# Kernel optimization log

Hardware: AMD Instinct MI355X
Metric: run time of the kernel (lower is better)

Reference implementation:

```python
import jax, jax.numpy as jnp
import numpy as np

KS = 5
STRIDE = 1


def extract_patches(x, ks, s):
    # TF tf.image.extract_patches ordering: (row, col, channel) flattened
    B, H, W, C = x.shape
    oh = (H - ks) // s + 1
    ow = (W - ks) // s + 1
    cols = [x[:, i:i + (oh - 1) * s + 1:s, j:j + (ow - 1) * s + 1:s, :]
            for i in range(ks) for j in range(ks)]
    p = jnp.stack(cols, axis=3)  # [B, oh, ow, ks*ks, C]
    return p.reshape(B, oh * ow, ks * ks * C)


def setup_inputs() -> dict:
    key = jax.random.key(0)
    k1, k2, k3 = jax.random.split(key, 3)
    B, H, W, C, K = 32, 14, 14, 32, 64
    mu_in = jax.random.normal(k1, (B, H, W, C), dtype=jnp.float32)
    Sigma_in = jax.random.uniform(k2, (B, H * W, H * W, C), dtype=jnp.float32)
    w_mu = 0.05 * jax.random.normal(k3, (KS, KS, C, K), dtype=jnp.float32)
    w_sigma = jnp.full((K,), -2.2, dtype=jnp.float32)
    return {"mu_in": mu_in, "Sigma_in": Sigma_in, "w_mu": w_mu, "w_sigma": w_sigma}


def reference(mu_in, Sigma_in, w_mu, w_sigma):
    B, H, W, C = mu_in.shape
    ks = w_mu.shape[0]
    K = w_mu.shape[-1]
    s = STRIDE

    # mean path: standard conv2d, NHWC / HWIO
    mu_out = jax.lax.conv_general_dilated(
        mu_in, w_mu, (s, s), 'VALID',
        dimension_numbers=('NHWC', 'HWIO', 'NHWC'))

    # diag of Sigma_in over the two N dims: [B,N,N,C] -> [B,C,N] -> [B,H,W,C]
    diag_sigma = jnp.diagonal(Sigma_in, axis1=1, axis2=2)           # [B,C,N]
    diag_sigma = jnp.transpose(diag_sigma, (0, 2, 1)).reshape(B, H, W, C)

    dsg = extract_patches(diag_sigma, ks, s)                        # [B,P,M]
    P = dsg.shape[1]

    mu_cov_sq = (w_mu * w_mu).reshape(-1, K)                        # [M,K]
    v1 = dsg @ mu_cov_sq                                            # [B,P,K]

    sp = jnp.log1p(jnp.exp(w_sigma))                                # softplus, [K]
    tr = jnp.sum(dsg, axis=2, keepdims=True)                        # [B,P,1]
    diag_vals = v1 + sp[None, None, :] * tr                         # [B,P,K] (trace1 + mu_wT_sigmags_mu_w diags)

    mu_p = extract_patches(mu_in, ks, s)                            # [B,P,M]
    G = jnp.einsum('bpm,bqm->bpq', mu_p, mu_p)                      # [B,P,P]

    Sigma_out = sp[None, None, None, :] * G[..., None]              # [B,P,P,K]
    ip = jnp.arange(P)
    Sigma_out = Sigma_out.at[:, ip, ip, :].add(diag_vals)

    Sigma_out = jnp.where(jnp.isnan(Sigma_out), 0.0, Sigma_out)
    Sigma_out = jnp.where(jnp.isinf(Sigma_out), 0.0, Sigma_out)

    # TF set_diag acts on the LAST two dims ([P,K] inner matrices) -- reproduce exactly
    m = min(P, K)
    ii = jnp.arange(m)
    Sigma_out = Sigma_out.at[:, :, ii, ii].set(jnp.abs(Sigma_out[:, :, ii, ii]))
    return mu_out, Sigma_out
```

## Files before the change

kernel.cpp:

```cpp
#include <hip/hip_runtime.h>
#include <cmath>

typedef __attribute__((ext_vector_type(8))) short short8;
typedef __attribute__((ext_vector_type(4))) float f32x4;

#define NB 32
#define MU_OUT_SZ (NB*100*64)
#define LDAP 56

#define WS_WF 0
#define WS_G  204800
#define WS_DV 1484800

__device__ inline unsigned short f2bf(float f) {
  unsigned u = __builtin_bit_cast(unsigned, f);
  u += 0x7fffu + ((u >> 16) & 1u);
  return (unsigned short)(u >> 16);
}

__global__ __launch_bounds__(256) void prepW(
    const float* __restrict__ w_mu, const float* __restrict__ w_sigma,
    unsigned short* __restrict__ wf) {
  const int wid = blockIdx.x * 256 + threadIdx.x;
  const int kind = wid >= 6400 ? 1 : 0;
  const int fid = kind ? wid - 6400 : wid;
  const int ij = fid >> 8;
  const int rest = fid & 255;
  const int n = rest >> 6, l = rest & 63;
  const int col = n * 16 + (l & 15);
  const int m0 = ij * 32 + (l >> 4) * 8;
  const float sp = log1pf(expf(w_sigma[col]));
  unsigned short v[8];
#pragma unroll
  for (int i = 0; i < 8; ++i) {
    float wv = w_mu[(m0 + i) * 64 + col];
    float x = kind ? (wv * wv + sp) : wv;
    v[i] = f2bf(x);
  }
  uint4 pk;
  pk.x = v[0] | ((unsigned)v[1] << 16);
  pk.y = v[2] | ((unsigned)v[3] << 16);
  pk.z = v[4] | ((unsigned)v[5] << 16);
  pk.w = v[6] | ((unsigned)v[7] << 16);
  *(uint4*)(wf + (size_t)((ij * 8 + kind * 4 + n) * 64 + l) * 8) = pk;
}

__global__ __launch_bounds__(256) void gemm(
    const float* __restrict__ mu_in, const float* __restrict__ Sigma_in,
    const unsigned short* __restrict__ wf,
    float* __restrict__ G, float* __restrict__ dv, float* __restrict__ out) {
  __shared__ unsigned short mu_sh[196 * LDAP];
  __shared__ unsigned short sd_sh[196 * LDAP];
  const int r = blockIdx.x;
  const int b = blockIdx.y;
  const int t = threadIdx.x, l = t & 63, w = t >> 6;

  const float4* mu4 = (const float4*)(mu_in + (size_t)b * 6272);
  for (int f = t; f < 1568; f += 256) {
    const float4 v = mu4[f];
    const int row = f >> 3, c = (f & 7) * 4;
    ushort4 pv;
    pv.x = f2bf(v.x); pv.y = f2bf(v.y); pv.z = f2bf(v.z); pv.w = f2bf(v.w);
    *(ushort4*)(mu_sh + row * LDAP + c) = pv;
    const float4 s = *(const float4*)(Sigma_in +
        ((size_t)(b * 196 + row) * 196 + row) * 32 + c);
    ushort4 ps;
    ps.x = f2bf(s.x); ps.y = f2bf(s.y); ps.z = f2bf(s.z); ps.w = f2bf(s.w);
    *(ushort4*)(sd_sh + row * LDAP + c) = ps;
  }
  __syncthreads();

  const int laneP = l & 15, g16 = (l >> 4) * 8;
  int pA = r * 16 + laneP; if (pA > 99) pA = 99;
  const int baseA = ((pA / 10) * 14 + (pA % 10)) * LDAP + g16;
  const int prow0 = (l >> 4) * 4;

  if (w <= 1) {
    const int c0 = w * 4;
    int baseB[4];
#pragma unroll
    for (int i = 0; i < 4; ++i) {
      int col = (c0 + i) * 16 + laneP;
      int pc = col > 99 ? 99 : col;
      baseB[i] = ((pc / 10) * 14 + (pc % 10)) * LDAP + g16;
    }
    f32x4 acc[4] = {};
#pragma unroll
    for (int ij = 0; ij < 25; ++ij) {
      const int off = ((ij / 5) * 14 + (ij % 5)) * LDAP;
      const short8 fA = *(const short8*)(mu_sh + baseA + off);
#pragma unroll
      for (int i = 0; i < 4; ++i) {
        const short8 fB = *(const short8*)(mu_sh + baseB[i] + off);
        acc[i] = __builtin_amdgcn_mfma_f32_16x16x32_bf16(fA, fB, acc[i], 0, 0, 0);
      }
    }
    float* Gb = G + (size_t)b * 10000;
#pragma unroll
    for (int i = 0; i < 4; ++i) {
      const int col = (c0 + i) * 16 + laneP;
      if (col < 100) {
#pragma unroll
        for (int j = 0; j < 4; ++j) {
          const int row = r * 16 + prow0 + j;
          if (row < 100) Gb[row * 100 + col] = acc[i][j];
        }
      }
    }
  } else if (w == 2) {
    f32x4 acc[4] = {};
#pragma unroll
    for (int ij = 0; ij < 25; ++ij) {
      const int off = ((ij / 5) * 14 + (ij % 5)) * LDAP;
      const short8 fA = *(const short8*)(mu_sh + baseA + off);
#pragma unroll
      for (int n = 0; n < 4; ++n) {
        const short8 bw = *(const short8*)(wf + (size_t)((ij * 8 + n) * 64 + l) * 8);
        acc[n] = __builtin_amdgcn_mfma_f32_16x16x32_bf16(fA, bw, acc[n], 0, 0, 0);
      }
    }
    float* mo = out + (size_t)b * 6400;
#pragma unroll
    for (int n = 0; n < 4; ++n) {
      const int k = n * 16 + laneP;
#pragma unroll
      for (int j = 0; j < 4; ++j) {
        const int p = r * 16 + prow0 + j;
        if (p < 100) mo[p * 64 + k] = acc[n][j];
      }
    }
  } else {
    f32x4 acc[4] = {};
#pragma unroll
    for (int ij = 0; ij < 25; ++ij) {
      const int off = ((ij / 5) * 14 + (ij % 5)) * LDAP;
      const short8 fS = *(const short8*)(sd_sh + baseA + off);
#pragma unroll
      for (int n = 0; n < 4; ++n) {
        const short8 b2 = *(const short8*)(wf + (size_t)((ij * 8 + 4 + n) * 64 + l) * 8);
        acc[n] = __builtin_amdgcn_mfma_f32_16x16x32_bf16(fS, b2, acc[n], 0, 0, 0);
      }
    }
    float* dvb = dv + (size_t)b * 6400;
#pragma unroll
    for (int n = 0; n < 4; ++n) {
      const int k = n * 16 + laneP;
#pragma unroll
      for (int j = 0; j < 4; ++j) {
        const int p = r * 16 + prow0 + j;
        if (p < 100) dvb[p * 64 + k] = acc[n][j];
      }
    }
  }
}

__global__ __launch_bounds__(256) void writer(
    const float* __restrict__ G, const float* __restrict__ dv,
    const float* __restrict__ w_sigma, float* __restrict__ out) {
  const unsigned tid = blockIdx.x * 256 + threadIdx.x;
  const int k4 = (tid & 15) * 4;
  const float4 wsv = *(const float4*)(w_sigma + k4);
  f32x4 sp4;
  sp4.x = log1pf(expf(wsv.x));
  sp4.y = log1pf(expf(wsv.y));
  sp4.z = log1pf(expf(wsv.z));
  sp4.w = log1pf(expf(wsv.w));
  float* sig = out + MU_OUT_SZ;
  for (unsigned l4 = tid; l4 < 5120000u; l4 += 524288u) {
    const unsigned rr = l4 >> 4;
    const unsigned q = rr % 100u;
    const unsigned pq = rr / 100u;
    const unsigned p = pq % 100u;
    const float g = G[rr];
    f32x4 v;
    v.x = sp4.x * g; v.y = sp4.y * g; v.z = sp4.z * g; v.w = sp4.w * g;
    if (q == p) {
      const float4 dvv = *(const float4*)(dv + (size_t)pq * 64 + k4);
      v.x += dvv.x; v.y += dvv.y; v.z += dvv.z; v.w += dvv.w;
    }
    v.x = (q == (unsigned)k4)     ? fabsf(v.x) : v.x;
    v.y = (q == (unsigned)k4 + 1) ? fabsf(v.y) : v.y;
    v.z = (q == (unsigned)k4 + 2) ? fabsf(v.z) : v.z;
    v.w = (q == (unsigned)k4 + 3) ? fabsf(v.w) : v.w;
    __builtin_nontemporal_store(v, (f32x4*)(sig + (size_t)l4 * 4));
  }
}

extern "C" void kernel_launch(void* const* d_in, const int* in_sizes, int n_in,
                              void* d_out, int out_size, void* d_ws, size_t ws_size,
                              hipStream_t stream) {
  const float* mu_in    = (const float*)d_in[0];
  const float* Sigma_in = (const float*)d_in[1];
  const float* w_mu     = (const float*)d_in[2];
  const float* w_sigma  = (const float*)d_in[3];
  float* out = (float*)d_out;
  unsigned char* ws = (unsigned char*)d_ws;
  unsigned short* wf = (unsigned short*)(ws + WS_WF);
  float* G  = (float*)(ws + WS_G);
  float* dv = (float*)(ws + WS_DV);

  prepW<<<50, 256, 0, stream>>>(w_mu, w_sigma, wf);
  gemm<<<dim3(7, NB), 256, 0, stream>>>(mu_in, Sigma_in, wf, G, dv, out);
  writer<<<2048, 256, 0, stream>>>(G, dv, w_sigma, out);
}
```

Before: 37.00 us.

## Spread gemm MFMA work across eight waves and stage prepW weights in LDS

The gemm kernel grows from 4 to 8 waves per block. Each wave now owns one 16-column G tile plus one mu_out or diag-variance tile, instead of four tiles each, and weight fragments are prefetched one step ahead. prepW loads each 5x5 tap's weights into shared memory with coalesced float4 reads, then packs both bf16 variants from there. This shortens the serial MFMA chain per wave and raises wave-level parallelism, but the gemm is a small slice next to the writer kernel, which is bound by output bandwidth.

```diff
diff --git a/kernel.cpp b/kernel.cpp
--- a/kernel.cpp
+++ b/kernel.cpp
@@ -21,31 +21,38 @@
 __global__ __launch_bounds__(256) void prepW(
     const float* __restrict__ w_mu, const float* __restrict__ w_sigma,
     unsigned short* __restrict__ wf) {
-  const int wid = blockIdx.x * 256 + threadIdx.x;
-  const int kind = wid >= 6400 ? 1 : 0;
-  const int fid = kind ? wid - 6400 : wid;
-  const int ij = fid >> 8;
-  const int rest = fid & 255;
-  const int n = rest >> 6, l = rest & 63;
-  const int col = n * 16 + (l & 15);
-  const int m0 = ij * 32 + (l >> 4) * 8;
-  const float sp = log1pf(expf(w_sigma[col]));
-  unsigned short v[8];
+  __shared__ float wsh[2048];
+  const int ij = blockIdx.x, t = threadIdx.x;
+  const float4* src = (const float4*)(w_mu + (size_t)ij * 2048);
+  ((float4*)wsh)[t]       = src[t];
+  ((float4*)wsh)[t + 256] = src[t + 256];
+  __syncthreads();
 #pragma unroll
-  for (int i = 0; i < 8; ++i) {
-    float wv = w_mu[(m0 + i) * 64 + col];
-    float x = kind ? (wv * wv + sp) : wv;
-    v[i] = f2bf(x);
+  for (int id0 = 0; id0 < 512; id0 += 256) {
+    const int id = id0 + t;
+    const int kind = id >> 8;
+    const int rest = id & 255;
+    const int n = rest >> 6, l = rest & 63;
+    const int col = n * 16 + (l & 15);
+    const int m0 = (l >> 4) * 8;
+    const float sp = log1pf(expf(w_sigma[col]));
+    unsigned short v[8];
+#pragma unroll
+    for (int i = 0; i < 8; ++i) {
+      const float wv = wsh[(m0 + i) * 64 + col];
+      const float x = kind ? (wv * wv + sp) : wv;
+      v[i] = f2bf(x);
+    }
+    uint4 pk;
+    pk.x = v[0] | ((unsigned)v[1] << 16);
+    pk.y = v[2] | ((unsigned)v[3] << 16);
+    pk.z = v[4] | ((unsigned)v[5] << 16);
+    pk.w = v[6] | ((unsigned)v[7] << 16);
+    *(uint4*)(wf + (size_t)((ij * 8 + kind * 4 + n) * 64 + l) * 8) = pk;
   }
-  uint4 pk;
-  pk.x = v[0] | ((unsigned)v[1] << 16);
-  pk.y = v[2] | ((unsigned)v[3] << 16);
-  pk.z = v[4] | ((unsigned)v[5] << 16);
-  pk.w = v[6] | ((unsigned)v[7] << 16);
-  *(uint4*)(wf + (size_t)((ij * 8 + kind * 4 + n) * 64 + l) * 8) = pk;
 }
 
-__global__ __launch_bounds__(256) void gemm(
+__global__ __launch_bounds__(512) void gemm(
     const float* __restrict__ mu_in, const float* __restrict__ Sigma_in,
     const unsigned short* __restrict__ wf,
     float* __restrict__ G, float* __restrict__ dv, float* __restrict__ out) {
@@ -56,7 +63,7 @@
   const int t = threadIdx.x, l = t & 63, w = t >> 6;
 
   const float4* mu4 = (const float4*)(mu_in + (size_t)b * 6272);
-  for (int f = t; f < 1568; f += 256) {
+  for (int f = t; f < 1568; f += 512) {
     const float4 v = mu4[f];
     const int row = f >> 3, c = (f & 7) * 4;
     ushort4 pv;
@@ -71,85 +78,62 @@
   __syncthreads();
 
   const int laneP = l & 15, g16 = (l >> 4) * 8;
-  int pA = r * 16 + laneP; if (pA > 99) pA = 99;
+  const int pA = (r * 16 + laneP > 99) ? 99 : r * 16 + laneP;
   const int baseA = ((pA / 10) * 14 + (pA % 10)) * LDAP + g16;
+  const bool doG = (w < 7);
+  const int q = w * 16 + laneP;
+  const int qc = q > 99 ? 99 : q;
+  const int baseB = ((qc / 10) * 14 + (qc % 10)) * LDAP + g16;
+  const bool doMu = (w < 4);
+  const int n = doMu ? w : (w - 4);
+  const int kslot = doMu ? n : (4 + n);
+
+  const short8* wfp = (const short8*)wf;
+  short8 fw = wfp[(size_t)kslot * 64 + l];
+  f32x4 aG = {}, aX = {};
+  for (int ij = 0; ij < 25; ++ij) {
+    const short8 fw_n = (ij < 24) ? wfp[(size_t)((ij + 1) * 8 + kslot) * 64 + l] : fw;
+    const int off = ((ij / 5) * 14 + (ij % 5)) * LDAP;
+    if (doG) {
+      const short8 fA = *(const short8*)(mu_sh + baseA + off);
+      const short8 fB = *(const short8*)(mu_sh + baseB + off);
+      aG = __builtin_amdgcn_mfma_f32_16x16x32_bf16(fA, fB, aG, 0, 0, 0);
+      if (doMu) {
+        aX = __builtin_amdgcn_mfma_f32_16x16x32_bf16(fA, fw, aX, 0, 0, 0);
+      } else {
+        const short8 fS = *(const short8*)(sd_sh + baseA + off);
+        aX = __builtin_amdgcn_mfma_f32_16x16x32_bf16(fS, fw, aX, 0, 0, 0);
+      }
+    } else {
+      const short8 fS = *(const short8*)(sd_sh + baseA + off);
+      aX = __builtin_amdgcn_mfma_f32_16x16x32_bf16(fS, fw, aX, 0, 0, 0);
+    }
+    fw = fw_n;
+  }
+
   const int prow0 = (l >> 4) * 4;
-
-  if (w <= 1) {
-    const int c0 = w * 4;
-    int baseB[4];
-#pragma unroll
-    for (int i = 0; i < 4; ++i) {
-      int col = (c0 + i) * 16 + laneP;
-      int pc = col > 99 ? 99 : col;
-      baseB[i] = ((pc / 10) * 14 + (pc % 10)) * LDAP + g16;
-    }
-    f32x4 acc[4] = {};
-#pragma unroll
-    for (int ij = 0; ij < 25; ++ij) {
-      const int off = ((ij / 5) * 14 + (ij % 5)) * LDAP;
-      const short8 fA = *(const short8*)(mu_sh + baseA + off);
-#pragma unroll
-      for (int i = 0; i < 4; ++i) {
-        const short8 fB = *(const short8*)(mu_sh + baseB[i] + off);
-        acc[i] = __builtin_amdgcn_mfma_f32_16x16x32_bf16(fA, fB, acc[i], 0, 0, 0);
-      }
-    }
+  if (doG && q < 100) {
     float* Gb = G + (size_t)b * 10000;
 #pragma unroll
-    for (int i = 0; i < 4; ++i) {
-      const int col = (c0 + i) * 16 + laneP;
-      if (col < 100) {
-#pragma unroll
-        for (int j = 0; j < 4; ++j) {
-          const int row = r * 16 + prow0 + j;
-          if (row < 100) Gb[row * 100 + col] = acc[i][j];
-        }
-      }
+    for (int j = 0; j < 4; ++j) {
+      const int row = r * 16 + prow0 + j;
+      if (row < 100) Gb[row * 100 + q] = aG[j];
     }
-  } else if (w == 2) {
-    f32x4 acc[4] = {};
-#pragma unroll
-    for (int ij = 0; ij < 25; ++ij) {
-      const int off = ((ij / 5) * 14 + (ij % 5)) * LDAP;
-      const short8 fA = *(const short8*)(mu_sh + baseA + off);
-#pragma unroll
-      for (int n = 0; n < 4; ++n) {
-        const short8 bw = *(const short8*)(wf + (size_t)((ij * 8 + n) * 64 + l) * 8);
-        acc[n] = __builtin_amdgcn_mfma_f32_16x16x32_bf16(fA, bw, acc[n], 0, 0, 0);
-      }
-    }
+  }
+  const int k = n * 16 + laneP;
+  if (doMu) {
     float* mo = out + (size_t)b * 6400;
 #pragma unroll
-    for (int n = 0; n < 4; ++n) {
-      const int k = n * 16 + laneP;
-#pragma unroll
-      for (int j = 0; j < 4; ++j) {
-        const int p = r * 16 + prow0 + j;
-        if (p < 100) mo[p * 64 + k] = acc[n][j];
-      }
+    for (int j = 0; j < 4; ++j) {
+      const int p = r * 16 + prow0 + j;
+      if (p < 100) mo[p * 64 + k] = aX[j];
     }
   } else {
-    f32x4 acc[4] = {};
-#pragma unroll
-    for (int ij = 0; ij < 25; ++ij) {
-      const int off = ((ij / 5) * 14 + (ij % 5)) * LDAP;
-      const short8 fS = *(const short8*)(sd_sh + baseA + off);
-#pragma unroll
-      for (int n = 0; n < 4; ++n) {
-        const short8 b2 = *(const short8*)(wf + (size_t)((ij * 8 + 4 + n) * 64 + l) * 8);
-        acc[n] = __builtin_amdgcn_mfma_f32_16x16x32_bf16(fS, b2, acc[n], 0, 0, 0);
-      }
-    }
     float* dvb = dv + (size_t)b * 6400;
 #pragma unroll
-    for (int n = 0; n < 4; ++n) {
-      const int k = n * 16 + laneP;
-#pragma unroll
-      for (int j = 0; j < 4; ++j) {
-        const int p = r * 16 + prow0 + j;
-        if (p < 100) dvb[p * 64 + k] = acc[n][j];
-      }
+    for (int j = 0; j < 4; ++j) {
+      const int p = r * 16 + prow0 + j;
+      if (p < 100) dvb[p * 64 + k] = aX[j];
     }
   }
 }
@@ -199,7 +183,7 @@
   float* G  = (float*)(ws + WS_G);
   float* dv = (float*)(ws + WS_DV);
 
-  prepW<<<50, 256, 0, stream>>>(w_mu, w_sigma, wf);
-  gemm<<<dim3(7, NB), 256, 0, stream>>>(mu_in, Sigma_in, wf, G, dv, out);
+  prepW<<<25, 256, 0, stream>>>(w_mu, w_sigma, wf);
+  gemm<<<dim3(7, NB), 512, 0, stream>>>(mu_in, Sigma_in, wf, G, dv, out);
   writer<<<2048, 256, 0, stream>>>(G, dv, w_sigma, out);
 }
```

Result: faster. 33.42 us (-9.7%).
